# Performance work log

Measured on AMD Instinct MI355X. Metric: run time of the kernel, lower is better.

Reference implementation:

```python
import math
import jax, jax.numpy as jnp
import numpy as np

B, H, L, E = 32, 8, 2048, 64  # D == E required by the gather in time_delay_agg_full
FACTOR = 1


def setup_inputs() -> dict:
    key = jax.random.key(0)
    kq, kk, kv = jax.random.split(key, 3)
    return {
        "queries": jax.random.normal(kq, (B, H, L, E), dtype=jnp.float32),
        "keys": jax.random.normal(kk, (B, H, L, E), dtype=jnp.float32),
        "values": jax.random.normal(kv, (B, H, L, E), dtype=jnp.float32),
    }


def _time_delay_agg_full(values, corr, factor=FACTOR):
    # values, corr: [B, H, L, D]; aggregation (roll + weighted sum) along last dim D
    length = values.shape[-1]
    top_k = int(factor * math.log(length))
    weights, delay = jax.lax.top_k(corr, top_k)          # [B,H,L,K]
    tmp_corr = jax.nn.softmax(weights, axis=-1)          # [B,H,L,K]
    init_index = jnp.arange(length)                      # [D]
    delays_agg = jnp.zeros_like(values)
    # K is small (int(log(D)) = 4): fixed-size loop, each iter a circular gather
    for i in range(top_k):
        idx = (init_index + delay[..., i:i + 1]) % length            # [B,H,L,D]
        pattern = jnp.take_along_axis(values, idx, axis=-1)         # [B,H,L,D]
        delays_agg = delays_agg + pattern * tmp_corr[..., i:i + 1]
    return delays_agg


def reference(queries, keys, values):
    Bq, Hq, Lq, Eq = queries.shape
    S = values.shape[2]
    # L == S in our setup; replicate the truncation branch faithfully
    values = values[:, :, :Lq, :]
    keys = keys[:, :, :Lq, :]
    # FFT-based autocorrelation along the feature dim (last axis)
    q_fft = jnp.fft.fft(queries, axis=-1)
    k_fft = jnp.fft.fft(keys, axis=-1)
    res = q_fft * jnp.conj(k_fft)
    # torch.fft.irfft crops the complex input to n//2+1 bins; numpy/jax irfft does the same
    corr = jnp.fft.irfft(res, n=Eq, axis=-1)             # [B,H,L,E] float
    V = _time_delay_agg_full(values, corr)
    return V, jnp.transpose(corr, (0, 3, 1, 2))
```

## Files before the change

### kernel.cpp

```cpp
#include <hip/hip_runtime.h>
#include <cmath>

#define NB 32
#define NH 8
#define NL 2048
#define NE 64

__global__ __launch_bounds__(256, 4) void autocorr_kernel(
    const float* __restrict__ qg_,
    const float* __restrict__ kg_,
    const float* __restrict__ vg_,
    float* __restrict__ outV,
    float* __restrict__ outC)
{
    __shared__ alignas(16) float qb[64][64];
    __shared__ alignas(16) float kk[64][64];
    __shared__ float        cval[64][17];
    __shared__ unsigned int cidx4[64][5];
    __shared__ float        wts[64][5];
    __shared__ unsigned int dpack[64];

    const int tid  = threadIdx.x;
    const int tile = blockIdx.x & 31;
    const int bh   = blockIdx.x >> 5;
    const int b    = bh >> 3;
    const int h    = bh & 7;
    const int l0   = tile * 64;
    const size_t rowbase = (size_t)bh * NL + l0;

    const float4* q4 = (const float4*)(qg_ + rowbase * NE);
    const float4* k4 = (const float4*)(kg_ + rowbase * NE);
    const float4* v4 = (const float4*)(vg_ + rowbase * NE);

    #pragma unroll
    for (int i = 0; i < 4; i++) {
        int idx = tid + i * 256;
        int r = idx >> 4, g = idx & 15;
        int gs = (g ^ (r & 7)) * 4;
        float4 qv = q4[idx];
        float4 kv = k4[idx];
        *(float4*)&qb[r][gs] = qv;
        *(float4*)&kk[r][gs] = kv;
    }
    __syncthreads();

    const int wv = tid >> 6;
    const int r  = tid & 63;
    const int d0 = wv * 16;
    const int rq = r & 7;

    float acc[16];
    #pragma unroll
    for (int u = 0; u < 16; u++) acc[u] = 0.f;

    const float* qrow = &qb[r][0];
    const float* krow = &kk[r][0];

    #pragma unroll
    for (int c = 0; c < 64; c += 16) {
        float qv[16];
        #pragma unroll
        for (int i = 0; i < 4; i++) {
            float4 t = *(const float4*)(qrow + (((c >> 2) + i) ^ rq) * 4);
            qv[i*4+0]=t.x; qv[i*4+1]=t.y; qv[i*4+2]=t.z; qv[i*4+3]=t.w;
        }
        float kv[32];
        const int gs0 = (64 + c - d0 - 16) >> 2;
        #pragma unroll
        for (int i = 0; i < 8; i++) {
            float4 t = *(const float4*)(krow + ((((gs0 + i) & 15) ^ rq) * 4));
            kv[i*4+0]=t.x; kv[i*4+1]=t.y; kv[i*4+2]=t.z; kv[i*4+3]=t.w;
        }
        #pragma unroll
        for (int u = 0; u < 16; u++) {
            #pragma unroll
            for (int tt = 0; tt < 16; tt++) {
                acc[u] = fmaf(qv[tt], kv[tt - u + 16], acc[u]);
            }
        }
    }

    {
        float* oc = outC + ((size_t)(b * NE + d0) * NH + h) * NL + l0 + r;
        #pragma unroll
        for (int u = 0; u < 16; u++) {
            oc[(size_t)u * (NH * NL)] = acc[u];
        }
    }

    float bv[4] = {-3.0e38f, -3.0e38f, -3.0e38f, -3.0e38f};
    int   bi[4] = {0, 0, 0, 0};
    #pragma unroll
    for (int u = 0; u < 16; u++) {
        float x = acc[u]; int ix = d0 + u;
        if (x > bv[3]) {
            if (x > bv[1]) {
                if (x > bv[0]) { bv[3]=bv[2];bi[3]=bi[2]; bv[2]=bv[1];bi[2]=bi[1]; bv[1]=bv[0];bi[1]=bi[0]; bv[0]=x; bi[0]=ix; }
                else           { bv[3]=bv[2];bi[3]=bi[2]; bv[2]=bv[1];bi[2]=bi[1]; bv[1]=x; bi[1]=ix; }
            } else {
                if (x > bv[2]) { bv[3]=bv[2];bi[3]=bi[2]; bv[2]=x; bi[2]=ix; }
                else           { bv[3]=x; bi[3]=ix; }
            }
        }
    }
    #pragma unroll
    for (int j = 0; j < 4; j++) cval[r][wv*4 + j] = bv[j];
    cidx4[r][wv] = (unsigned int)bi[0] | ((unsigned int)bi[1] << 8)
                 | ((unsigned int)bi[2] << 16) | ((unsigned int)bi[3] << 24);
    __syncthreads();

    #pragma unroll
    for (int i = 0; i < 4; i++) {
        int idx = tid + i * 256;
        int rr = idx >> 4, g = idx & 15;
        int gr = ((g + (rr & 7)) & 15) * 4;
        *(float4*)&qb[rr][gr] = v4[idx];
    }
    if (tid < 64) {
        float mv[4] = {-3.0e38f, -3.0e38f, -3.0e38f, -3.0e38f};
        int   mi[4] = {0, 0, 0, 0};
        #pragma unroll
        for (int w4 = 0; w4 < 4; w4++) {
            unsigned int ip = cidx4[tid][w4];
            #pragma unroll
            for (int j = 0; j < 4; j++) {
                float x = cval[tid][w4*4 + j];
                int ix = (int)((ip >> (8*j)) & 255u);
                if (x > mv[3]) {
                    if (x > mv[1]) {
                        if (x > mv[0]) { mv[3]=mv[2];mi[3]=mi[2]; mv[2]=mv[1];mi[2]=mi[1]; mv[1]=mv[0];mi[1]=mi[0]; mv[0]=x; mi[0]=ix; }
                        else           { mv[3]=mv[2];mi[3]=mi[2]; mv[2]=mv[1];mi[2]=mi[1]; mv[1]=x; mi[1]=ix; }
                    } else {
                        if (x > mv[2]) { mv[3]=mv[2];mi[3]=mi[2]; mv[2]=x; mi[2]=ix; }
                        else           { mv[3]=x; mi[3]=ix; }
                    }
                }
            }
        }
        float m = mv[0];
        float e0 = __expf(mv[0]-m), e1 = __expf(mv[1]-m), e2 = __expf(mv[2]-m), e3 = __expf(mv[3]-m);
        float inv = 1.0f / (e0 + e1 + e2 + e3);
        wts[tid][0]=e0*inv; wts[tid][1]=e1*inv; wts[tid][2]=e2*inv; wts[tid][3]=e3*inv;
        dpack[tid] = (unsigned int)mi[0] | ((unsigned int)mi[1] << 8)
                   | ((unsigned int)mi[2] << 16) | ((unsigned int)mi[3] << 24);
    }
    __syncthreads();

    {
        const int rr = tid >> 2;
        const int j0 = (tid & 3) * 16;
        const int rot = (rr & 7) * 4;
        const unsigned int dp = dpack[rr];
        float w[4]; int dl[4];
        #pragma unroll
        for (int i = 0; i < 4; i++) { w[i] = wts[rr][i]; dl[i] = (int)((dp >> (8*i)) & 63u); }
        float o[16];
        #pragma unroll
        for (int jj = 0; jj < 16; jj++) o[jj] = 0.f;
        #pragma unroll
        for (int i = 0; i < 4; i++) {
            int s = (j0 + dl[i] + rot) & 63;
            #pragma unroll
            for (int jj = 0; jj < 16; jj++) {
                o[jj] = fmaf(w[i], qb[rr][(s + jj) & 63], o[jj]);
            }
        }
        float* ov = outV + (rowbase + rr) * NE + j0;
        #pragma unroll
        for (int i = 0; i < 4; i++) {
            float4 t; t.x = o[i*4+0]; t.y = o[i*4+1]; t.z = o[i*4+2]; t.w = o[i*4+3];
            *(float4*)&ov[i*4] = t;
        }
    }
}

extern "C" void kernel_launch(void* const* d_in, const int* in_sizes, int n_in,
                              void* d_out, int out_size, void* d_ws, size_t ws_size,
                              hipStream_t stream) {
    const float* q = (const float*)d_in[0];
    const float* k = (const float*)d_in[1];
    const float* v = (const float*)d_in[2];
    float* outV = (float*)d_out;
    float* outC = outV + (size_t)NB * NH * NL * NE;
    dim3 grid(NB * NH * (NL / 64));
    autocorr_kernel<<<grid, 256, 0, stream>>>(q, k, v, outV, outC);
}
```

Before: 509.6 us.

## Cache K row in registers and gather V directly from global memory

```diff
diff --git a/kernel.cpp b/kernel.cpp
--- a/kernel.cpp
+++ b/kernel.cpp
@@ -17,7 +17,7 @@
     __shared__ alignas(16) float kk[64][64];
     __shared__ float        cval[64][17];
     __shared__ unsigned int cidx4[64][5];
-    __shared__ float        wts[64][5];
+    __shared__ float4       wts4[64];
     __shared__ unsigned int dpack[64];
 
     const int tid  = threadIdx.x;
@@ -30,7 +30,6 @@
 
     const float4* q4 = (const float4*)(qg_ + rowbase * NE);
     const float4* k4 = (const float4*)(kg_ + rowbase * NE);
-    const float4* v4 = (const float4*)(vg_ + rowbase * NE);
 
     #pragma unroll
     for (int i = 0; i < 4; i++) {
@@ -49,33 +48,37 @@
     const int d0 = wv * 16;
     const int rq = r & 7;
 
+    float kreg[64];
+    {
+        const float* krow = &kk[r][0];
+        #pragma unroll
+        for (int m = 0; m < 16; m++) {
+            int g = (((m - 4 * wv) & 15) ^ rq) * 4;
+            float4 t = *(const float4*)(krow + g);
+            kreg[4*m+0]=t.x; kreg[4*m+1]=t.y; kreg[4*m+2]=t.z; kreg[4*m+3]=t.w;
+        }
+    }
+
     float acc[16];
     #pragma unroll
     for (int u = 0; u < 16; u++) acc[u] = 0.f;
 
-    const float* qrow = &qb[r][0];
-    const float* krow = &kk[r][0];
-
-    #pragma unroll
-    for (int c = 0; c < 64; c += 16) {
-        float qv[16];
+    {
+        const float* qrow = &qb[r][0];
         #pragma unroll
-        for (int i = 0; i < 4; i++) {
-            float4 t = *(const float4*)(qrow + (((c >> 2) + i) ^ rq) * 4);
-            qv[i*4+0]=t.x; qv[i*4+1]=t.y; qv[i*4+2]=t.z; qv[i*4+3]=t.w;
-        }
-        float kv[32];
-        const int gs0 = (64 + c - d0 - 16) >> 2;
-        #pragma unroll
-        for (int i = 0; i < 8; i++) {
-            float4 t = *(const float4*)(krow + ((((gs0 + i) & 15) ^ rq) * 4));
-            kv[i*4+0]=t.x; kv[i*4+1]=t.y; kv[i*4+2]=t.z; kv[i*4+3]=t.w;
-        }
-        #pragma unroll
-        for (int u = 0; u < 16; u++) {
+        for (int c = 0; c < 64; c += 16) {
+            float qv[16];
             #pragma unroll
-            for (int tt = 0; tt < 16; tt++) {
-                acc[u] = fmaf(qv[tt], kv[tt - u + 16], acc[u]);
+            for (int i = 0; i < 4; i++) {
+                float4 t = *(const float4*)(qrow + (((c >> 2) + i) ^ rq) * 4);
+                qv[i*4+0]=t.x; qv[i*4+1]=t.y; qv[i*4+2]=t.z; qv[i*4+3]=t.w;
+            }
+            #pragma unroll
+            for (int u = 0; u < 16; u++) {
+                #pragma unroll
+                for (int tt = 0; tt < 16; tt++) {
+                    acc[u] = fmaf(qv[tt], kreg[(c + tt - u) & 63], acc[u]);
+                }
             }
         }
     }
@@ -109,13 +112,6 @@
                  | ((unsigned int)bi[2] << 16) | ((unsigned int)bi[3] << 24);
     __syncthreads();
 
-    #pragma unroll
-    for (int i = 0; i < 4; i++) {
-        int idx = tid + i * 256;
-        int rr = idx >> 4, g = idx & 15;
-        int gr = ((g + (rr & 7)) & 15) * 4;
-        *(float4*)&qb[rr][gr] = v4[idx];
-    }
     if (tid < 64) {
         float mv[4] = {-3.0e38f, -3.0e38f, -3.0e38f, -3.0e38f};
         int   mi[4] = {0, 0, 0, 0};
@@ -140,36 +136,33 @@
         float m = mv[0];
         float e0 = __expf(mv[0]-m), e1 = __expf(mv[1]-m), e2 = __expf(mv[2]-m), e3 = __expf(mv[3]-m);
         float inv = 1.0f / (e0 + e1 + e2 + e3);
-        wts[tid][0]=e0*inv; wts[tid][1]=e1*inv; wts[tid][2]=e2*inv; wts[tid][3]=e3*inv;
+        float4 w; w.x = e0*inv; w.y = e1*inv; w.z = e2*inv; w.w = e3*inv;
+        wts4[tid] = w;
         dpack[tid] = (unsigned int)mi[0] | ((unsigned int)mi[1] << 8)
                    | ((unsigned int)mi[2] << 16) | ((unsigned int)mi[3] << 24);
     }
     __syncthreads();
 
     {
-        const int rr = tid >> 2;
-        const int j0 = (tid & 3) * 16;
-        const int rot = (rr & 7) * 4;
-        const unsigned int dp = dpack[rr];
-        float w[4]; int dl[4];
+        const int lane = tid & 63;
+        const float* vbase = vg_ + rowbase * NE;
+        float* obase = outV + rowbase * NE;
         #pragma unroll
-        for (int i = 0; i < 4; i++) { w[i] = wts[rr][i]; dl[i] = (int)((dp >> (8*i)) & 63u); }
-        float o[16];
-        #pragma unroll
-        for (int jj = 0; jj < 16; jj++) o[jj] = 0.f;
-        #pragma unroll
-        for (int i = 0; i < 4; i++) {
-            int s = (j0 + dl[i] + rot) & 63;
-            #pragma unroll
-            for (int jj = 0; jj < 16; jj++) {
-                o[jj] = fmaf(w[i], qb[rr][(s + jj) & 63], o[jj]);
-            }
-        }
-        float* ov = outV + (rowbase + rr) * NE + j0;
-        #pragma unroll
-        for (int i = 0; i < 4; i++) {
-            float4 t; t.x = o[i*4+0]; t.y = o[i*4+1]; t.z = o[i*4+2]; t.w = o[i*4+3];
-            *(float4*)&ov[i*4] = t;
+        for (int t = 0; t < 16; t++) {
+            const int rr = wv * 16 + t;
+            float4 w4 = wts4[rr];
+            unsigned int dp = dpack[rr];
+            const float* vr = vbase + rr * NE;
+            int dl0 = (int)(dp & 63u);
+            int dl1 = (int)((dp >> 8) & 63u);
+            int dl2 = (int)((dp >> 16) & 63u);
+            int dl3 = (int)((dp >> 24) & 63u);
+            float o;
+            o = w4.x * vr[(lane + dl0) & 63];
+            o = fmaf(w4.y, vr[(lane + dl1) & 63], o);
+            o = fmaf(w4.z, vr[(lane + dl2) & 63], o);
+            o = fmaf(w4.w, vr[(lane + dl3) & 63], o);
+            obase[rr * NE + lane] = o;
         }
     }
 }
```

After: 515.9 us. About the same (+1.2%).
